# Performance work log

Measured on AMD Instinct MI355X. Metric: run time of the kernel, lower is better.

## Reference

```python
import jax, jax.numpy as jnp
import numpy as np

B, T, E, WIN, OC, VOCAB = 256, 2048, 128, 5, 128, 50000


def setup_inputs() -> dict:
    key = jax.random.key(0)
    k1, k2, k3, k4, k5, k6 = jax.random.split(key, 6)
    return {
        "x": jax.random.randint(k1, (B, T), 0, VOCAB + 1, dtype=jnp.int32),
        "emb_table": jax.random.normal(k2, (VOCAB + 1, E), dtype=jnp.float32),
        "att_w": jax.random.normal(k3, (WIN, E), dtype=jnp.float32) * 0.05,
        "att_b": jax.random.normal(k4, (1,), dtype=jnp.float32),
        "cnn_w": jax.random.normal(k5, (OC, E), dtype=jnp.float32) * 0.05,
        "cnn_b": jax.random.normal(k6, (OC,), dtype=jnp.float32),
    }


def reference(x, emb_table, att_w, att_b, cnn_w, cnn_b):
    win = att_w.shape[0]
    pad = (win - 1) // 2
    embed = emb_table[x]                                   # [B, T, E]
    x_pad = jnp.pad(embed, ((0, 0), (pad, pad), (0, 0)))
    T_ = embed.shape[1]
    # Sliding-window dot product over full embed dim (the degenerate Conv2d)
    s = jnp.zeros(embed.shape[:2], dtype=embed.dtype)      # [B, T]
    for k in range(win):
        s = s + jnp.einsum('bte,e->bt', x_pad[:, k:k + T_, :], att_w[k])
    scores = jax.nn.sigmoid(s + att_b[0])                  # [B, T]
    gated = embed * scores[:, :, None]                     # [B, T, E]
    feat = jnp.tanh(jnp.einsum('bte,oe->bto', gated, cnn_w) + cnn_b)  # [B, T, OC]
    out = jnp.max(feat, axis=1)                            # [B, OC] (maxpool over seq)
    return out[:, :, None, None]                           # [B, OC, 1, 1]
```

## Files before the change

### kernel.cpp

```cpp
#include <hip/hip_runtime.h>
#include <hip/hip_bf16.h>
#include <math.h>

#define B_   256
#define T_   2048
#define E_   128
#define WIN_ 5
#define PAD_ 2
#define OC_  128
#define VOCAB1 50001
#define NT   8
#define TT   64
#define BTOK (NT * TT)
#define REAL_ROWS (TT + WIN_ - 1)
#define ROWS 80
#define ASTR 136

#define NTAB_CH (VOCAB1 * E_ / 8)

typedef __attribute__((ext_vector_type(8))) short short8;
typedef __attribute__((ext_vector_type(4))) float floatx4;

static __device__ __forceinline__ short f2bf(float f) {
    union { __hip_bfloat16 h; short s; } u;
    u.h = __float2bfloat16(f);
    return u.s;
}

__device__ __forceinline__ void atomicMaxFloat(float* addr, float v) {
    if (v >= 0.0f) atomicMax((int*)addr, __float_as_int(v));
    else           atomicMin((unsigned int*)addr, __float_as_uint(v));
}

__device__ __forceinline__ void conv_chunk(long i, const float* __restrict__ emb,
                                           const float* __restrict__ cnn_w,
                                           const float* __restrict__ att_w,
                                           short* __restrict__ tab, short* __restrict__ wsw,
                                           short* __restrict__ wsatt) {
    const float* src;
    short* dst;
    if (i < NTAB_CH) { src = emb; dst = tab; }
    else if ((i -= NTAB_CH) < OC_ * E_ / 8) { src = cnn_w; dst = wsw; }
    else if ((i -= OC_ * E_ / 8) < WIN_ * E_ / 8) { src = att_w; dst = wsatt; }
    else return;
    const float4* s = (const float4*)src + (size_t)i * 2;
    float4 a = s[0], b = s[1];
    short8 o = { f2bf(a.x), f2bf(a.y), f2bf(a.z), f2bf(a.w),
                 f2bf(b.x), f2bf(b.y), f2bf(b.z), f2bf(b.w) };
    *(short8*)(dst + (size_t)i * 8) = o;
}

__global__ void prep_full(const float* __restrict__ emb, const float* __restrict__ cnn_w,
                          const float* __restrict__ att_w,
                          short* __restrict__ tab, short* __restrict__ wsw,
                          short* __restrict__ wsatt) {
    long i = (long)(blockIdx.x * 256 + threadIdx.x) * 2;
    conv_chunk(i,     emb, cnn_w, att_w, tab, wsw, wsatt);
    conv_chunk(i + 1, emb, cnn_w, att_w, tab, wsw, wsatt);
}

__global__ void prep_small(const float* __restrict__ cnn_w, const float* __restrict__ att_w,
                           short* __restrict__ wsw, short* __restrict__ wsatt) {
    int i = blockIdx.x * 256 + threadIdx.x;
    if (i < OC_ * E_)  wsw[i]   = f2bf(cnn_w[i]);
    if (i < WIN_ * E_) wsatt[i] = f2bf(att_w[i]);
}

template <bool TAB_BF16>
__launch_bounds__(256, 4)
__global__ void local_attn_main(const int* __restrict__ x,
                                const short* __restrict__ tab,
                                const float* __restrict__ emb,
                                const float* __restrict__ att_b_p,
                                const short* __restrict__ wsw,
                                const short* __restrict__ wsatt,
                                const float* __restrict__ cnn_b,
                                float* __restrict__ out) {
    __shared__ short sh_a[ROWS * ASTR];
    __shared__ short sh_att[16 * ASTR];
    __shared__ float sh_r[ROWS * 8];
    __shared__ float sh_score[TT];
    __shared__ int   sh_idx[NT * ROWS];

    const int tid  = threadIdx.x;
    const int lane = tid & 63;
    const int w    = tid >> 6;
    const int b    = blockIdx.y;
    const int t0   = blockIdx.x * BTOK;
    const int l15  = lane & 15;
    const int quad = lane >> 4;
    const int rbase = tid >> 4;
    const int c     = tid & 15;

    for (int i = tid; i < NT * ROWS; i += 256) {
        int tile = i / ROWS, row = i - tile * ROWS;
        int t = t0 + tile * TT + row - PAD_;
        sh_idx[i] = (row < REAL_ROWS && t >= 0 && t < T_) ? x[b * T_ + t] : -1;
    }
    {
        int o = tid >> 4, cc = tid & 15;
        short8 v = (short8){0,0,0,0,0,0,0,0};
        if (o < WIN_) v = *(const short8*)(wsatt + o * E_ + cc * 8);
        *(short8*)(&sh_att[o * ASTR + cc * 8]) = v;
    }
    short8 Bf[2][4];
    #pragma unroll
    for (int j = 0; j < 2; j++)
        #pragma unroll
        for (int ks = 0; ks < 4; ks++)
            Bf[j][ks] = *(const short8*)(wsw + (size_t)(w * 32 + j * 16 + l15) * E_ + ks * 32 + quad * 8);
    __syncthreads();

    short8 g[5];
    #pragma unroll
    for (int k = 0; k < 5; k++) {
        int row = rbase + 16 * k;
        int idx = sh_idx[row];
        short8 v = (short8){0,0,0,0,0,0,0,0};
        if (idx >= 0) {
            if (TAB_BF16) v = *(const short8*)(tab + (size_t)idx * E_ + c * 8);
            else {
                const float4* p = (const float4*)(emb + (size_t)idx * E_ + c * 8);
                float4 p0 = p[0], p1 = p[1];
                v = (short8){ f2bf(p0.x), f2bf(p0.y), f2bf(p0.z), f2bf(p0.w),
                              f2bf(p1.x), f2bf(p1.y), f2bf(p1.z), f2bf(p1.w) };
            }
        }
        g[k] = v;
    }
    #pragma unroll
    for (int k = 0; k < 5; k++)
        *(short8*)(&sh_a[(rbase + 16 * k) * ASTR + c * 8]) = g[k];
    __syncthreads();

    const float attb = att_b_p[0];
    float mm[2] = { -INFINITY, -INFINITY };

    for (int it = 0; it < NT; it++) {
        for (int mt = w; mt < 5; mt += 4) {
            floatx4 acc = (floatx4){0.f, 0.f, 0.f, 0.f};
            #pragma unroll
            for (int ks = 0; ks < 4; ks++) {
                short8 a  = *(const short8*)(&sh_a[(mt * 16 + l15) * ASTR + ks * 32 + quad * 8]);
                short8 bs = *(const short8*)(&sh_att[l15 * ASTR + ks * 32 + quad * 8]);
                acc = __builtin_amdgcn_mfma_f32_16x16x32_bf16(a, bs, acc, 0, 0, 0);
            }
            if (l15 < 8) {
                #pragma unroll
                for (int r = 0; r < 4; r++)
                    sh_r[(mt * 16 + quad * 4 + r) * 8 + l15] = acc[r];
            }
        }
        __syncthreads();

        if (it + 1 < NT) {
            const int* idxp = &sh_idx[(it + 1) * ROWS];
            #pragma unroll
            for (int k = 0; k < 5; k++) {
                int idx = idxp[rbase + 16 * k];
                short8 v = (short8){0,0,0,0,0,0,0,0};
                if (idx >= 0) {
                    if (TAB_BF16) v = *(const short8*)(tab + (size_t)idx * E_ + c * 8);
                    else {
                        const float4* p = (const float4*)(emb + (size_t)idx * E_ + c * 8);
                        float4 p0 = p[0], p1 = p[1];
                        v = (short8){ f2bf(p0.x), f2bf(p0.y), f2bf(p0.z), f2bf(p0.w),
                                      f2bf(p1.x), f2bf(p1.y), f2bf(p1.z), f2bf(p1.w) };
                    }
                }
                g[k] = v;
            }
        }

        if (tid < TT) {
            float s = attb;
            #pragma unroll
            for (int k = 0; k < WIN_; k++) s += sh_r[(tid + k) * 8 + k];
            sh_score[tid] = 1.0f / (1.0f + __expf(-s));
        }

        floatx4 acc[4][2];
        #pragma unroll
        for (int i = 0; i < 4; i++)
            #pragma unroll
            for (int j = 0; j < 2; j++) acc[i][j] = (floatx4){0.f, 0.f, 0.f, 0.f};

        #pragma unroll
        for (int ks = 0; ks < 4; ks++) {
            int ko = ks * 32 + quad * 8;
            #pragma unroll
            for (int i = 0; i < 4; i++) {
                short8 ai = *(const short8*)(&sh_a[(PAD_ + i * 16 + l15) * ASTR + ko]);
                acc[i][0] = __builtin_amdgcn_mfma_f32_16x16x32_bf16(ai, Bf[0][ks], acc[i][0], 0, 0, 0);
                acc[i][1] = __builtin_amdgcn_mfma_f32_16x16x32_bf16(ai, Bf[1][ks], acc[i][1], 0, 0, 0);
            }
        }
        __syncthreads();

        #pragma unroll
        for (int i = 0; i < 4; i++) {
            #pragma unroll
            for (int r = 0; r < 4; r++) {
                float sc = sh_score[i * 16 + quad * 4 + r];
                mm[0] = fmaxf(mm[0], sc * acc[i][0][r]);
                mm[1] = fmaxf(mm[1], sc * acc[i][1][r]);
            }
        }

        if (it + 1 < NT) {
            #pragma unroll
            for (int k = 0; k < 5; k++)
                *(short8*)(&sh_a[(rbase + 16 * k) * ASTR + c * 8]) = g[k];
            __syncthreads();
        }
    }

    #pragma unroll
    for (int j = 0; j < 2; j++) {
        float m = mm[j];
        m = fmaxf(m, __shfl_xor(m, 16));
        m = fmaxf(m, __shfl_xor(m, 32));
        if (lane < 16) {
            int o = w * 32 + j * 16 + lane;
            atomicMaxFloat(&out[b * OC_ + o], tanhf(m + cnn_b[o]));
        }
    }
}

extern "C" void kernel_launch(void* const* d_in, const int* in_sizes, int n_in,
                              void* d_out, int out_size, void* d_ws, size_t ws_size,
                              hipStream_t stream) {
    const int*   x     = (const int*)d_in[0];
    const float* emb   = (const float*)d_in[1];
    const float* att_w = (const float*)d_in[2];
    const float* att_b = (const float*)d_in[3];
    const float* cnn_w = (const float*)d_in[4];
    const float* cnn_b = (const float*)d_in[5];
    float* out = (float*)d_out;

    hipMemsetAsync(d_out, 0xFF, (size_t)B_ * OC_ * sizeof(float), stream);

    const size_t tab_elems = (size_t)VOCAB1 * E_;
    const size_t need = tab_elems * 2 + OC_ * E_ * 2 + WIN_ * E_ * 2 + 64;

    dim3 grid(T_ / BTOK, B_);

    if (ws_size >= need) {
        short* tab    = (short*)d_ws;
        short* ws_w   = tab + tab_elems;
        short* ws_att = ws_w + OC_ * E_;
        long total = (NTAB_CH + OC_ * E_ / 8 + WIN_ * E_ / 8 + 1) / 2;
        prep_full<<<(int)((total + 255) / 256), 256, 0, stream>>>(emb, cnn_w, att_w, tab, ws_w, ws_att);
        local_attn_main<true><<<grid, 256, 0, stream>>>(x, tab, emb, att_b, ws_w, ws_att, cnn_b, out);
    } else {
        short* ws_w   = (short*)d_ws;
        short* ws_att = ws_w + OC_ * E_;
        prep_small<<<16, 256, 0, stream>>>(cnn_w, att_w, ws_w, ws_att);
        local_attn_main<false><<<grid, 256, 0, stream>>>(x, (const short*)nullptr, emb, att_b, ws_w, ws_att, cnn_b, out);
    }
}
```

Baseline: 127.0 us.

## Split fused kernel into score pass and register-pipelined gather GEMM-max pass

The fused kernel is split into two kernels. The first computes sigmoid attention scores per token and writes them to a workspace buffer. The second gathers bf16 embedding rows straight into MFMA A-fragments in registers, prefetching the next chunk, and applies the stored scores before the max reduction. This removes shared-memory staging and the per-tile __syncthreads from the main GEMM, at the cost of an extra launch, a second gather of the embedding table and a B*T score round-trip through global memory.

```diff
diff --git a/kernel.cpp b/kernel.cpp
--- a/kernel.cpp
+++ b/kernel.cpp
@@ -9,12 +9,11 @@
 #define PAD_ 2
 #define OC_  128
 #define VOCAB1 50001
-#define NT   8
 #define TT   64
-#define BTOK (NT * TT)
 #define REAL_ROWS (TT + WIN_ - 1)
 #define ROWS 80
 #define ASTR 136
+#define MCH  8
 
 #define NTAB_CH (VOCAB1 * E_ / 8)
 
@@ -59,6 +58,164 @@
     conv_chunk(i + 1, emb, cnn_w, att_w, tab, wsw, wsatt);
 }
 
+__launch_bounds__(256, 4)
+__global__ void score_kernel(const int* __restrict__ x,
+                             const short* __restrict__ tab,
+                             const float* __restrict__ att_b_p,
+                             const short* __restrict__ wsatt,
+                             float* __restrict__ scores) {
+    __shared__ short sh_a[ROWS * ASTR];
+    __shared__ short sh_att[16 * ASTR];
+    __shared__ float sh_r[ROWS * 8];
+    __shared__ int   sh_idx[ROWS];
+
+    const int tid  = threadIdx.x;
+    const int lane = tid & 63;
+    const int w    = tid >> 6;
+    const int b    = blockIdx.y;
+    const int t0   = blockIdx.x * TT;
+    const int l15  = lane & 15;
+    const int quad = lane >> 4;
+    const int rbase = tid >> 4;
+    const int c     = tid & 15;
+
+    if (tid < ROWS) {
+        int gt = t0 + tid - PAD_;
+        sh_idx[tid] = (tid < REAL_ROWS && gt >= 0 && gt < T_) ? x[b * T_ + gt] : -1;
+    }
+    {
+        int o = tid >> 4, cc = tid & 15;
+        short8 v = (short8){0,0,0,0,0,0,0,0};
+        if (o < WIN_) v = *(const short8*)(wsatt + o * E_ + cc * 8);
+        *(short8*)(&sh_att[o * ASTR + cc * 8]) = v;
+    }
+    __syncthreads();
+
+    #pragma unroll
+    for (int k = 0; k < 5; k++) {
+        int row = rbase + 16 * k;
+        int idx = sh_idx[row];
+        short8 v = (short8){0,0,0,0,0,0,0,0};
+        if (idx >= 0) v = *(const short8*)(tab + (size_t)idx * E_ + c * 8);
+        *(short8*)(&sh_a[row * ASTR + c * 8]) = v;
+    }
+    __syncthreads();
+
+    for (int mt = w; mt < 5; mt += 4) {
+        floatx4 acc = (floatx4){0.f, 0.f, 0.f, 0.f};
+        #pragma unroll
+        for (int ks = 0; ks < 4; ks++) {
+            short8 a  = *(const short8*)(&sh_a[(mt * 16 + l15) * ASTR + ks * 32 + quad * 8]);
+            short8 bs = *(const short8*)(&sh_att[l15 * ASTR + ks * 32 + quad * 8]);
+            acc = __builtin_amdgcn_mfma_f32_16x16x32_bf16(a, bs, acc, 0, 0, 0);
+        }
+        if (l15 < 8) {
+            #pragma unroll
+            for (int r = 0; r < 4; r++)
+                sh_r[(mt * 16 + quad * 4 + r) * 8 + l15] = acc[r];
+        }
+    }
+    __syncthreads();
+
+    if (tid < TT) {
+        float s = att_b_p[0];
+        #pragma unroll
+        for (int k = 0; k < WIN_; k++) s += sh_r[(tid + k) * 8 + k];
+        scores[b * T_ + t0 + tid] = 1.0f / (1.0f + __expf(-s));
+    }
+}
+
+__launch_bounds__(256, 3)
+__global__ void gemm_max(const int* __restrict__ x,
+                         const short* __restrict__ tab,
+                         const float* __restrict__ scores,
+                         const short* __restrict__ wsw,
+                         const float* __restrict__ cnn_b,
+                         float* __restrict__ out) {
+    const int tid  = threadIdx.x;
+    const int lane = tid & 63;
+    const int w    = tid >> 6;
+    const int tsub = w & 1;
+    const int h    = w >> 1;
+    const int b    = blockIdx.y;
+    const int tbase = blockIdx.x * 256 + tsub * 128;
+    const int l15  = lane & 15;
+    const int quad = lane >> 4;
+    const int koff = quad * 8;
+
+    short8 Bf[4][4];
+    #pragma unroll
+    for (int j = 0; j < 4; j++)
+        #pragma unroll
+        for (int ks = 0; ks < 4; ks++)
+            Bf[j][ks] = *(const short8*)(wsw + (size_t)(h * 64 + j * 16 + l15) * E_ + ks * 32 + koff);
+
+    const int* xrow = x + b * T_ + tbase;
+    const float* srow = scores + b * T_ + tbase;
+
+    float mm[4] = { -INFINITY, -INFINITY, -INFINITY, -INFINITY };
+
+    int idx_n = xrow[l15];
+    short8 Acur[4];
+    {
+        const short* rp = tab + (size_t)idx_n * E_ + koff;
+        Acur[0] = *(const short8*)(rp);
+        Acur[1] = *(const short8*)(rp + 32);
+        Acur[2] = *(const short8*)(rp + 64);
+        Acur[3] = *(const short8*)(rp + 96);
+    }
+    float4 sc_cur = *(const float4*)(srow + quad * 4);
+    idx_n = xrow[16 + l15];
+
+    #pragma unroll
+    for (int cch = 0; cch < MCH; cch++) {
+        short8 Anx[4];
+        float4 sc_nx;
+        if (cch + 1 < MCH) {
+            const short* rp = tab + (size_t)idx_n * E_ + koff;
+            Anx[0] = *(const short8*)(rp);
+            Anx[1] = *(const short8*)(rp + 32);
+            Anx[2] = *(const short8*)(rp + 64);
+            Anx[3] = *(const short8*)(rp + 96);
+            sc_nx = *(const float4*)(srow + (cch + 1) * 16 + quad * 4);
+            if (cch + 2 < MCH) idx_n = xrow[(cch + 2) * 16 + l15];
+        }
+
+        floatx4 acc[4];
+        #pragma unroll
+        for (int j = 0; j < 4; j++) acc[j] = (floatx4){0.f, 0.f, 0.f, 0.f};
+        #pragma unroll
+        for (int ks = 0; ks < 4; ks++)
+            #pragma unroll
+            for (int j = 0; j < 4; j++)
+                acc[j] = __builtin_amdgcn_mfma_f32_16x16x32_bf16(Acur[ks], Bf[j][ks], acc[j], 0, 0, 0);
+
+        float scr[4] = { sc_cur.x, sc_cur.y, sc_cur.z, sc_cur.w };
+        #pragma unroll
+        for (int j = 0; j < 4; j++)
+            #pragma unroll
+            for (int r = 0; r < 4; r++)
+                mm[j] = fmaxf(mm[j], scr[r] * acc[j][r]);
+
+        if (cch + 1 < MCH) {
+            #pragma unroll
+            for (int k = 0; k < 4; k++) Acur[k] = Anx[k];
+            sc_cur = sc_nx;
+        }
+    }
+
+    #pragma unroll
+    for (int j = 0; j < 4; j++) {
+        float m = mm[j];
+        m = fmaxf(m, __shfl_xor(m, 16));
+        m = fmaxf(m, __shfl_xor(m, 32));
+        if (lane < 16) {
+            int o = h * 64 + j * 16 + lane;
+            atomicMaxFloat(&out[b * OC_ + o], tanhf(m + cnn_b[o]));
+        }
+    }
+}
+
 __global__ void prep_small(const float* __restrict__ cnn_w, const float* __restrict__ att_w,
                            short* __restrict__ wsw, short* __restrict__ wsatt) {
     int i = blockIdx.x * 256 + threadIdx.x;
@@ -66,33 +223,31 @@
     if (i < WIN_ * E_) wsatt[i] = f2bf(att_w[i]);
 }
 
-template <bool TAB_BF16>
 __launch_bounds__(256, 4)
-__global__ void local_attn_main(const int* __restrict__ x,
-                                const short* __restrict__ tab,
-                                const float* __restrict__ emb,
-                                const float* __restrict__ att_b_p,
-                                const short* __restrict__ wsw,
-                                const short* __restrict__ wsatt,
-                                const float* __restrict__ cnn_b,
-                                float* __restrict__ out) {
+__global__ void fallback_main(const int* __restrict__ x,
+                              const float* __restrict__ emb,
+                              const float* __restrict__ att_b_p,
+                              const short* __restrict__ wsw,
+                              const short* __restrict__ wsatt,
+                              const float* __restrict__ cnn_b,
+                              float* __restrict__ out) {
     __shared__ short sh_a[ROWS * ASTR];
     __shared__ short sh_att[16 * ASTR];
     __shared__ float sh_r[ROWS * 8];
     __shared__ float sh_score[TT];
-    __shared__ int   sh_idx[NT * ROWS];
+    __shared__ int   sh_idx[8 * ROWS];
 
     const int tid  = threadIdx.x;
     const int lane = tid & 63;
     const int w    = tid >> 6;
     const int b    = blockIdx.y;
-    const int t0   = blockIdx.x * BTOK;
+    const int t0   = blockIdx.x * (8 * TT);
     const int l15  = lane & 15;
     const int quad = lane >> 4;
     const int rbase = tid >> 4;
     const int c     = tid & 15;
 
-    for (int i = tid; i < NT * ROWS; i += 256) {
+    for (int i = tid; i < 8 * ROWS; i += 256) {
         int tile = i / ROWS, row = i - tile * ROWS;
         int t = t0 + tile * TT + row - PAD_;
         sh_idx[i] = (row < REAL_ROWS && t >= 0 && t < T_) ? x[b * T_ + t] : -1;
@@ -114,17 +269,13 @@
     short8 g[5];
     #pragma unroll
     for (int k = 0; k < 5; k++) {
-        int row = rbase + 16 * k;
-        int idx = sh_idx[row];
+        int idx = sh_idx[rbase + 16 * k];
         short8 v = (short8){0,0,0,0,0,0,0,0};
         if (idx >= 0) {
-            if (TAB_BF16) v = *(const short8*)(tab + (size_t)idx * E_ + c * 8);
-            else {
-                const float4* p = (const float4*)(emb + (size_t)idx * E_ + c * 8);
-                float4 p0 = p[0], p1 = p[1];
-                v = (short8){ f2bf(p0.x), f2bf(p0.y), f2bf(p0.z), f2bf(p0.w),
-                              f2bf(p1.x), f2bf(p1.y), f2bf(p1.z), f2bf(p1.w) };
-            }
+            const float4* p = (const float4*)(emb + (size_t)idx * E_ + c * 8);
+            float4 p0 = p[0], p1 = p[1];
+            v = (short8){ f2bf(p0.x), f2bf(p0.y), f2bf(p0.z), f2bf(p0.w),
+                          f2bf(p1.x), f2bf(p1.y), f2bf(p1.z), f2bf(p1.w) };
         }
         g[k] = v;
     }
@@ -136,7 +287,7 @@
     const float attb = att_b_p[0];
     float mm[2] = { -INFINITY, -INFINITY };
 
-    for (int it = 0; it < NT; it++) {
+    for (int it = 0; it < 8; it++) {
         for (int mt = w; mt < 5; mt += 4) {
             floatx4 acc = (floatx4){0.f, 0.f, 0.f, 0.f};
             #pragma unroll
@@ -153,20 +304,17 @@
         }
         __syncthreads();
 
-        if (it + 1 < NT) {
+        if (it + 1 < 8) {
             const int* idxp = &sh_idx[(it + 1) * ROWS];
             #pragma unroll
             for (int k = 0; k < 5; k++) {
                 int idx = idxp[rbase + 16 * k];
                 short8 v = (short8){0,0,0,0,0,0,0,0};
                 if (idx >= 0) {
-                    if (TAB_BF16) v = *(const short8*)(tab + (size_t)idx * E_ + c * 8);
-                    else {
-                        const float4* p = (const float4*)(emb + (size_t)idx * E_ + c * 8);
-                        float4 p0 = p[0], p1 = p[1];
-                        v = (short8){ f2bf(p0.x), f2bf(p0.y), f2bf(p0.z), f2bf(p0.w),
-                                      f2bf(p1.x), f2bf(p1.y), f2bf(p1.z), f2bf(p1.w) };
-                    }
+                    const float4* p = (const float4*)(emb + (size_t)idx * E_ + c * 8);
+                    float4 p0 = p[0], p1 = p[1];
+                    v = (short8){ f2bf(p0.x), f2bf(p0.y), f2bf(p0.z), f2bf(p0.w),
+                                  f2bf(p1.x), f2bf(p1.y), f2bf(p1.z), f2bf(p1.w) };
                 }
                 g[k] = v;
             }
@@ -184,7 +332,6 @@
         for (int i = 0; i < 4; i++)
             #pragma unroll
             for (int j = 0; j < 2; j++) acc[i][j] = (floatx4){0.f, 0.f, 0.f, 0.f};
-
         #pragma unroll
         for (int ks = 0; ks < 4; ks++) {
             int ko = ks * 32 + quad * 8;
@@ -207,7 +354,7 @@
             }
         }
 
-        if (it + 1 < NT) {
+        if (it + 1 < 8) {
             #pragma unroll
             for (int k = 0; k < 5; k++)
                 *(short8*)(&sh_a[(rbase + 16 * k) * ASTR + c * 8]) = g[k];
@@ -241,21 +388,25 @@
     hipMemsetAsync(d_out, 0xFF, (size_t)B_ * OC_ * sizeof(float), stream);
 
     const size_t tab_elems = (size_t)VOCAB1 * E_;
-    const size_t need = tab_elems * 2 + OC_ * E_ * 2 + WIN_ * E_ * 2 + 64;
-
-    dim3 grid(T_ / BTOK, B_);
+    const size_t need = tab_elems * 2 + OC_ * E_ * 2 + WIN_ * E_ * 2
+                      + (size_t)B_ * T_ * 4 + 64;
 
     if (ws_size >= need) {
         short* tab    = (short*)d_ws;
         short* ws_w   = tab + tab_elems;
         short* ws_att = ws_w + OC_ * E_;
+        float* scores = (float*)(ws_att + WIN_ * E_);
         long total = (NTAB_CH + OC_ * E_ / 8 + WIN_ * E_ / 8 + 1) / 2;
         prep_full<<<(int)((total + 255) / 256), 256, 0, stream>>>(emb, cnn_w, att_w, tab, ws_w, ws_att);
-        local_attn_main<true><<<grid, 256, 0, stream>>>(x, tab, emb, att_b, ws_w, ws_att, cnn_b, out);
+        dim3 sgrid(T_ / TT, B_);
+        score_kernel<<<sgrid, 256, 0, stream>>>(x, tab, att_b, ws_att, scores);
+        dim3 mgrid(T_ / 256, B_);
+        gemm_max<<<mgrid, 256, 0, stream>>>(x, tab, scores, ws_w, cnn_b, out);
     } else {
         short* ws_w   = (short*)d_ws;
         short* ws_att = ws_w + OC_ * E_;
         prep_small<<<16, 256, 0, stream>>>(cnn_w, att_w, ws_w, ws_att);
-        local_attn_main<false><<<grid, 256, 0, stream>>>(x, (const short*)nullptr, emb, att_b, ws_w, ws_att, cnn_b, out);
-    }
-}
+        dim3 grid(T_ / (8 * TT), B_);
+        fallback_main<<<grid, 256, 0, stream>>>(x, emb, att_b, ws_w, ws_att, cnn_b, out);
+    }
+}
```

Measured after the change: 211.5 us. +66.5%, slower.
